# Performance work log

Hardware: AMD Instinct MI355X
Metric: run time of the kernel (lower is better)

## Reference

```python
import jax, jax.numpy as jnp
import numpy as np

B, N, E, H, D, MS, FF = 4, 500, 128, 8, 16, 16, 512
SQRT_D = 4.0  # sqrt_qkv_dim
EPS = 1e-5


def setup_inputs() -> dict:
    key = jax.random.key(0)
    ks = jax.random.split(key, 26)
    u = lambda k, sh, s: jax.random.uniform(k, sh, jnp.float32, -s, s)
    inp = {
        "x_edges_values": jax.random.uniform(ks[0], (B, N, N), jnp.float32),
        "depot_node_demand": jax.random.uniform(ks[1], (B, N, 1), jnp.float32),
        "rand": jax.random.uniform(ks[2], (B, E), jnp.float32),
        # attention projections (no bias)
        "Wq": u(ks[3], (E, H * D), E ** -0.5),
        "Wk": u(ks[4], (E, H * D), E ** -0.5),
        "Wv": u(ks[5], (E, H * D), E ** -0.5),
        # mixed-score per-head MLP
        "mix1_w": u(ks[6], (H, 2, MS), 0.7071067811865476),
        "mix1_b": u(ks[7], (H, MS), 0.7071067811865476),
        "mix2_w": u(ks[8], (H, MS, 1), 0.25),
        "mix2_b": u(ks[9], (H, 1), 0.25),
        # multi_head_combine
        "Wo": u(ks[10], (H * D, E), (H * D) ** -0.5),
        "bo": u(ks[11], (E,), (H * D) ** -0.5),
        # feed-forward
        "W1": u(ks[12], (E, FF), E ** -0.5),
        "b1": u(ks[13], (FF,), E ** -0.5),
        "W2": u(ks[14], (FF, E), FF ** -0.5),
        "b2": u(ks[15], (E,), FF ** -0.5),
        # batch norms (affine)
        "bn1_g": jnp.ones((E,), jnp.float32),
        "bn1_b": jnp.zeros((E,), jnp.float32),
        "bn2_g": jnp.ones((E,), jnp.float32),
        "bn2_b": jnp.zeros((E,), jnp.float32),
        # demand / node embeddings
        "Wd": u(ks[16], (1, E), 1.0),
        "bd": u(ks[17], (E,), 1.0),
        "Wn": u(ks[18], (2 * E, E), (2 * E) ** -0.5),
        "bn_node": u(ks[19], (E,), (2 * E) ** -0.5),
    }
    return inp


def _batchnorm(x, g, b):
    # BatchNorm1d in training mode over flattened [B*N, E]
    x2 = x.reshape(-1, E)
    m = x2.mean(0)
    v = ((x2 - m) ** 2).mean(0)  # biased variance, as torch uses for normalization
    return (((x2 - m) / jnp.sqrt(v + EPS)) * g + b).reshape(x.shape)


def reference(x_edges_values, depot_node_demand, rand, Wq, Wk, Wv,
              mix1_w, mix1_b, mix2_w, mix2_b, Wo, bo, W1, b1, W2, b2,
              bn1_g, bn1_b, bn2_g, bn2_b, Wd, bd, Wn, bn_node):
    # seed embeddings: row_emb zeros, col_emb scattered one-hot from a random perm
    row_emb = jnp.zeros((B, N, E), jnp.float32)
    perm = jnp.argsort(rand, axis=1)                       # [B, E] (seed_cnt = E since N > E)
    idx = jnp.concatenate([perm, perm, perm, perm], 1)[:, :N]  # 3E <= N < 4E branch
    col_emb = jax.nn.one_hot(idx, E, dtype=jnp.float32)    # [B, N, E]

    heads = lambda x: x.reshape(B, N, H, D).transpose(0, 2, 1, 3)  # [B,H,N,D]
    q = heads(row_emb @ Wq)
    k = heads(col_emb @ Wk)
    v = heads(col_emb @ Wv)

    dot = jnp.einsum('bhnd,bhmd->bhnm', q, k) / SQRT_D        # [B,H,N,N]
    cost = jnp.broadcast_to(x_edges_values[:, None], (B, H, N, N))
    two = jnp.stack([dot, cost], axis=-1)                      # [B,H,N,N,2]
    ms1 = jax.nn.relu(jnp.einsum('bhnmt,hts->bhnms', two, mix1_w)
                      + mix1_b[None, :, None, None, :])        # [B,H,N,N,MS]
    ms2 = jnp.einsum('bhnms,hso->bhnmo', ms1, mix2_w)[..., 0] \
          + mix2_b[None, :, None, :]                           # [B,H,N,N]
    weights = jax.nn.softmax(ms2, axis=-1)
    out = jnp.einsum('bhnm,bhmd->bhnd', weights, v)
    out_concat = out.transpose(0, 2, 1, 3).reshape(B, N, H * D)

    multi_head_out = out_concat @ Wo + bo
    out1 = _batchnorm(row_emb + multi_head_out, bn1_g, bn1_b)
    ff = jax.nn.relu(out1 @ W1 + b1) @ W2 + b2
    out3 = _batchnorm(out1 + ff, bn2_g, bn2_b)

    demand_feature = depot_node_demand @ Wd + bd               # [B,N,E]
    node_feature = jnp.concatenate([out3, demand_feature], -1) @ Wn + bn_node
    return node_feature
```

## Files before the change

### kernel.cpp

```cpp
#include <hip/hip_runtime.h>
#include <hip/hip_bf16.h>


#define BN_EPS 1e-5f
#define WS_X1    256000
#define WS_X2    512000
#define WS_SUM1  768000
#define WS_SQ1   768128
#define WS_SUM2  768256
#define WS_SQ2   768384
#define WS_UV    768512
#define WS_C0V   768640

#define GEMM_BATCH8(WPTR, LDW, KIDX, ACT2D, ACC)                        \
  {                                                                     \
    float4 w[8];                                                        \
    _Pragma("unroll")                                                   \
    for (int u = 0; u < 8; ++u)                                         \
      w[u] = *(const float4*)((WPTR) + (size_t)((KIDX) + u) * (LDW));   \
    _Pragma("unroll")                                                   \
    for (int u = 0; u < 8; ++u) {                                       \
      _Pragma("unroll")                                                 \
      for (int r = 0; r < 4; ++r) {                                     \
        float a = ACT2D[r][u];                                          \
        ACC[r][0] = fmaf(a, w[u].x, ACC[r][0]);                         \
        ACC[r][1] = fmaf(a, w[u].y, ACC[r][1]);                         \
        ACC[r][2] = fmaf(a, w[u].z, ACC[r][2]);                         \
        ACC[r][3] = fmaf(a, w[u].w, ACC[r][3]);                         \
      }                                                                 \
    }                                                                   \
  }

#define LOAD_ACT8(SRC2D, KIDX, ACT2D)                                   \
  {                                                                     \
    _Pragma("unroll")                                                   \
    for (int r = 0; r < 4; ++r) {                                       \
      float4 x = *(const float4*)&SRC2D[r][(KIDX)];                     \
      float4 y = *(const float4*)&SRC2D[r][(KIDX) + 4];                 \
      ACT2D[r][0] = x.x; ACT2D[r][1] = x.y; ACT2D[r][2] = x.z;          \
      ACT2D[r][3] = x.w; ACT2D[r][4] = y.x; ACT2D[r][5] = y.y;          \
      ACT2D[r][6] = y.z; ACT2D[r][7] = y.w;                             \
    }                                                                   \
  }

#define GB8_R2(WPTR, LDW, KIDX, ACT2D, ACC)                             \
  {                                                                     \
    float4 w[8];                                                        \
    _Pragma("unroll")                                                   \
    for (int u = 0; u < 8; ++u)                                         \
      w[u] = *(const float4*)((WPTR) + (size_t)((KIDX) + u) * (LDW));   \
    _Pragma("unroll")                                                   \
    for (int u = 0; u < 8; ++u) {                                       \
      _Pragma("unroll")                                                 \
      for (int r = 0; r < 2; ++r) {                                     \
        float a = ACT2D[r][u];                                          \
        ACC[r][0] = fmaf(a, w[u].x, ACC[r][0]);                         \
        ACC[r][1] = fmaf(a, w[u].y, ACC[r][1]);                         \
        ACC[r][2] = fmaf(a, w[u].z, ACC[r][2]);                         \
        ACC[r][3] = fmaf(a, w[u].w, ACC[r][3]);                         \
      }                                                                 \
    }                                                                   \
  }

#define LD_AV2(SRC_ROW0, SRC_ROW1, KIDX, ACT2D)                         \
  {                                                                     \
    float4 x0 = *(const float4*)&(SRC_ROW0)[(KIDX)];                    \
    float4 y0 = *(const float4*)&(SRC_ROW0)[(KIDX) + 4];                \
    float4 x1 = *(const float4*)&(SRC_ROW1)[(KIDX)];                    \
    float4 y1 = *(const float4*)&(SRC_ROW1)[(KIDX) + 4];                \
    ACT2D[0][0]=x0.x; ACT2D[0][1]=x0.y; ACT2D[0][2]=x0.z; ACT2D[0][3]=x0.w; \
    ACT2D[0][4]=y0.x; ACT2D[0][5]=y0.y; ACT2D[0][6]=y0.z; ACT2D[0][7]=y0.w; \
    ACT2D[1][0]=x1.x; ACT2D[1][1]=x1.y; ACT2D[1][2]=x1.z; ACT2D[1][3]=x1.w; \
    ACT2D[1][4]=y1.x; ACT2D[1][5]=y1.y; ACT2D[1][6]=y1.z; ACT2D[1][7]=y1.w; \
  }

__global__ __launch_bounds__(512, 4) void k_attn(const float* __restrict__ cost,
                                                 const float* __restrict__ rnd,
                                                 const float* __restrict__ Wv,
                                                 const float* __restrict__ mix1w,
                                                 const float* __restrict__ mix1b,
                                                 const float* __restrict__ mix2w,
                                                 const float* __restrict__ mix2b,
                                                 const float* __restrict__ Wo,
                                                 const float* __restrict__ bo,
                                                 float* __restrict__ ws) {
  __shared__ float scost[4][512];
  __shared__ float2 lut[8 * 256];
  __shared__ float aw[32][132];
  __shared__ float soc[4][132];
  __shared__ float sP[8][512];
  __shared__ float svr[128];
  __shared__ int   sperm[128];
  __shared__ float mu[8][16], mr[8][16], mA[8], mB[8];
  __shared__ float sS[512], sQ[512];
  const int t = threadIdx.x;
  const int lane = t & 63;
  const int blk = blockIdx.x;
  const int row0 = blk * 4;
  const int b = blk / 125;

  {
    int rr = t >> 7, i4 = t & 127;
    *(float4*)&scost[rr][i4 * 4] = (i4 < 125)
        ? *(const float4*)(cost + (size_t)(row0 + rr) * 500 + i4 * 4)
        : float4{0.f, 0.f, 0.f, 0.f};
  }
  if (t < 128) svr[t] = rnd[b * 128 + t];
  __syncthreads();
  if (t < 128) {
    float vt = svr[t];
    int rank = 0;
    for (int j = 0; j < 128; ++j) {
      float vj = svr[j];
      rank += (vj < vt) || (vj == vt && j < t);
    }
    sperm[rank] = t;
    int h = t >> 4, s = t & 15;
    float w1  = mix1w[h * 32 + 16 + s];
    float b1v = mix1b[h * 16 + s];
    float w2  = mix2w[h * 16 + s];
    bool tiny = fabsf(w1) < 1e-20f;
    float us = tiny ? 0.f : 0.5f * w2 * fabsf(w1);
    float rs = tiny ? 0.f : -b1v / w1;
    float Ap = 0.5f * w2 * w1;
    float Bp = 0.5f * w2 * b1v + (tiny ? 0.5f * w2 * fabsf(b1v) : 0.f);
    mu[h][s] = us; mr[h][s] = rs;
#pragma unroll
    for (int off = 1; off < 16; off <<= 1) {
      Ap += __shfl_xor(Ap, off);
      Bp += __shfl_xor(Bp, off);
    }
    if (s == 0) { mA[h] = Ap; mB[h] = Bp + mix2b[h]; }
  }
  __syncthreads();
  float* traw = &sP[0][0];
  if (t < 257) {
    float x = (float)t * (1.f / 255.f);
    for (int h = 0; h < 8; ++h) {
      float g = fmaf(x, mA[h], mB[h]);
#pragma unroll
      for (int s = 0; s < 16; ++s)
        g = fmaf(fabsf(x - mr[h][s]), mu[h][s], g);
      traw[h * 257 + t] = __expf(g);
    }
  }
  __syncthreads();
#pragma unroll
  for (int p = 0; p < 4; ++p) {
    int e = t + p * 512;
    int h = e >> 8, i = e & 255;
    float a = traw[h * 257 + i];
    lut[e] = float2{a, traw[h * 257 + i + 1] - a};
  }
  __syncthreads();
  {
    const int wid = t >> 6;
    const int r  = wid & 3;
    const int h0 = (wid >> 2) * 4;
    float cv8[8];
#pragma unroll
    for (int ii = 0; ii < 8; ++ii) cv8[ii] = scost[r][ii * 64 + lane];
    for (int h = h0; h < h0 + 4; ++h) {
      const float2* lh = &lut[h * 256];
      float wsum = 0.f, a0 = 0.f, a1 = 0.f;
#pragma unroll
      for (int ii = 0; ii < 8; ++ii) {
        float u = cv8[ii] * 255.f;
        int i = (int)u;
        float f = u - (float)i;
        float2 td = lh[i];
        float e = fmaf(td.y, f, td.x);
        if (ii == 7 && lane >= 52) e = 0.f;
        wsum += e;
        if (ii & 1) a1 += e; else a0 += e;
      }
#pragma unroll
      for (int off = 32; off; off >>= 1) wsum += __shfl_xor(wsum, off);
      float inv = 1.f / wsum;
      aw[r * 8 + h][lane]      = a0 * inv;
      aw[r * 8 + h][64 + lane] = a1 * inv;
    }
  }
  __syncthreads();
  {
    const int c  = t & 127;
    const int jh = t >> 7;
    const int h  = c >> 4;
    float acc4[4] = {0.f, 0.f, 0.f, 0.f};
    for (int jb = jh * 32; jb < jh * 32 + 32; jb += 8) {
      int rows[8];
#pragma unroll
      for (int u = 0; u < 8; ++u) rows[u] = sperm[jb + u];
      float wv8[8];
#pragma unroll
      for (int u = 0; u < 8; ++u) wv8[u] = Wv[(size_t)rows[u] * 128 + c];
#pragma unroll
      for (int r = 0; r < 4; ++r) {
        float4 aa = *(const float4*)&aw[r * 8 + h][jb];
        float4 ab = *(const float4*)&aw[r * 8 + h][jb + 4];
        acc4[r] = fmaf(aa.x, wv8[0], acc4[r]);
        acc4[r] = fmaf(aa.y, wv8[1], acc4[r]);
        acc4[r] = fmaf(aa.z, wv8[2], acc4[r]);
        acc4[r] = fmaf(aa.w, wv8[3], acc4[r]);
        acc4[r] = fmaf(ab.x, wv8[4], acc4[r]);
        acc4[r] = fmaf(ab.y, wv8[5], acc4[r]);
        acc4[r] = fmaf(ab.z, wv8[6], acc4[r]);
        acc4[r] = fmaf(ab.w, wv8[7], acc4[r]);
      }
    }
#pragma unroll
    for (int r = 0; r < 4; ++r) sP[jh][r * 128 + c] = acc4[r];
  }
  __syncthreads();
  {
    int r = t >> 7, c = t & 127;
    soc[r][c] = sP[0][r * 128 + c] + sP[1][r * 128 + c] +
                sP[2][r * 128 + c] + sP[3][r * 128 + c];
  }
  __syncthreads();
  {
    const int cg  = (t & 31) * 4;
    const int seg = (t >> 5) & 7;
    const int rh  = t >> 8;
    const int k0  = seg * 16;
    float acc[2][4] = {};
    float av[2][8];
#pragma unroll
    for (int kb = 0; kb < 16; kb += 8) {
      LD_AV2(soc[rh * 2], soc[rh * 2 + 1], k0 + kb, av);
      GB8_R2(Wo + cg, 128, k0 + kb, av, acc);
    }
#pragma unroll
    for (int r = 0; r < 2; ++r)
      *(float4*)&sP[seg][(rh * 2 + r) * 128 + cg] = *(float4*)acc[r];
  }
  __syncthreads();
  {
    int r = t >> 7, col = t & 127;
    float x = bo[col];
#pragma unroll
    for (int sg = 0; sg < 8; ++sg) x += sP[sg][r * 128 + col];
    ws[WS_X1 + (size_t)(row0 + r) * 128 + col] = x;
    sS[t] = x; sQ[t] = x * x;
  }
  __syncthreads();
  if (t < 128) {
    atomicAdd(ws + WS_SUM1 + t, sS[t] + sS[t+128] + sS[t+256] + sS[t+384]);
    atomicAdd(ws + WS_SQ1 + t, sQ[t] + sQ[t+128] + sQ[t+256] + sQ[t+384]);
  }
}

__global__ __launch_bounds__(512) void k_ffn(const float* __restrict__ W1,
                                             const float* __restrict__ b1,
                                             const float* __restrict__ g1,
                                             const float* __restrict__ bb1,
                                             const float* __restrict__ W2,
                                             const float* __restrict__ b2,
                                             const float* __restrict__ Wn,
                                             const float* __restrict__ Wd,
                                             const float* __restrict__ bd,
                                             const float* __restrict__ bnn,
                                             float* __restrict__ ws) {
  __shared__ float o1[8][128];
  __shared__ float sY[8][512];
  __shared__ float sP2[8][8][128];
  __shared__ float sS[512], sQ[512];
  const int t = threadIdx.x;
  const int row0 = blockIdx.x * 8;
  const int c0 = t & 127;
  float m1 = ws[WS_SUM1 + c0] * 5e-4f;
  float v1 = ws[WS_SQ1 + c0] * 5e-4f - m1 * m1;
  float scv = g1[c0] * rsqrtf(v1 + BN_EPS);
  float shv = bb1[c0] - m1 * scv;
  {
    int r0 = t >> 7;
    o1[r0][c0]     = ws[WS_X1 + (size_t)(row0 + r0) * 128 + c0] * scv + shv;
    o1[r0 + 4][c0] = ws[WS_X1 + (size_t)(row0 + r0 + 4) * 128 + c0] * scv + shv;
  }
  __syncthreads();
  {
    const int cg   = (t & 127) * 4;
    const int kseg = (t >> 7) & 1;
    const int rh   = t >> 8;
    const int kb0  = kseg * 64;
    float acc[4][4] = {};
    float av[4][8];
#pragma unroll
    for (int k0 = 0; k0 < 64; k0 += 8) {
      LOAD_ACT8((o1 + rh * 4), kb0 + k0, av);
      GEMM_BATCH8(W1 + cg, 512, kb0 + k0, av, acc);
    }
    float* pf = &sP2[0][0][0];
    if (kseg == 1) {
#pragma unroll
      for (int r = 0; r < 4; ++r)
        *(float4*)(pf + (size_t)(rh * 4 + r) * 512 + cg) = *(float4*)acc[r];
    }
    __syncthreads();
    if (kseg == 0) {
      float4 bv = *(const float4*)(b1 + cg);
#pragma unroll
      for (int r = 0; r < 4; ++r) {
        float4 p = *(float4*)(pf + (size_t)(rh * 4 + r) * 512 + cg);
        float4 y = {fmaxf(acc[r][0] + p.x + bv.x, 0.f),
                    fmaxf(acc[r][1] + p.y + bv.y, 0.f),
                    fmaxf(acc[r][2] + p.z + bv.z, 0.f),
                    fmaxf(acc[r][3] + p.w + bv.w, 0.f)};
        *(float4*)&sY[rh * 4 + r][cg] = y;
      }
    }
  }
  __syncthreads();
  {
    const int cg   = (t & 31) * 4;
    const int kseg = (t >> 5) & 7;
    const int rh   = t >> 8;
    const int k0   = kseg * 64;
    float acc[4][4] = {};
    float av[4][8];
#pragma unroll
    for (int kb = 0; kb < 64; kb += 8) {
      LOAD_ACT8((sY + rh * 4), k0 + kb, av);
      GEMM_BATCH8(W2 + cg, 128, k0 + kb, av, acc);
    }
#pragma unroll
    for (int r = 0; r < 4; ++r)
      *(float4*)&sP2[kseg][rh * 4 + r][cg] = *(float4*)acc[r];
  }
  __syncthreads();
  float s = 0.f, q = 0.f;
#pragma unroll
  for (int pass = 0; pass < 2; ++pass) {
    int idx = t + pass * 512;
    int col = idx & 127, r = idx >> 7;
    float x = b2[col] + o1[r][col];
#pragma unroll
    for (int sg = 0; sg < 8; ++sg) x += sP2[sg][r][col];
    ws[WS_X2 + (size_t)(row0 + r) * 128 + col] = x;
    s += x; q = fmaf(x, x, q);
  }
  sS[t] = s; sQ[t] = q;
  __syncthreads();
  if (t < 128) {
    atomicAdd(ws + WS_SUM2 + t, sS[t] + sS[t+128] + sS[t+256] + sS[t+384]);
    atomicAdd(ws + WS_SQ2 + t, sQ[t] + sQ[t+128] + sQ[t+256] + sQ[t+384]);
  }
  if (blockIdx.x == 0) {
    const int g = t >> 7;
    float u = 0.f, cc = 0.f;
#pragma unroll 8
    for (int e = g * 32; e < g * 32 + 32; ++e) {
      float wn = Wn[(size_t)(128 + e) * 128 + c0];
      u  = fmaf(Wd[e], wn, u);
      cc = fmaf(bd[e], wn, cc);
    }
    float* red = &sY[0][0];
    red[g * 128 + c0] = u;
    red[512 + g * 128 + c0] = cc;
    __syncthreads();
    if (t < 128) {
      ws[WS_UV + t]  = red[t] + red[128 + t] + red[256 + t] + red[384 + t];
      ws[WS_C0V + t] = red[512 + t] + red[640 + t] + red[768 + t] +
                       red[896 + t] + bnn[t];
    }
  }
}

__global__ __launch_bounds__(512, 4) void k_final(const float* __restrict__ Wn,
                                                  const float* __restrict__ g2,
                                                  const float* __restrict__ bb2,
                                                  const float* __restrict__ dem,
                                                  float* __restrict__ out,
                                                  float* __restrict__ ws) {
  __shared__ float o3[4][132];
  __shared__ float sP[8][4][128];
  const int t = threadIdx.x;
  const int row0 = blockIdx.x * 4;
  const int c0 = t & 127;
  float m2 = ws[WS_SUM2 + c0] * 5e-4f;
  float v2 = ws[WS_SQ2 + c0] * 5e-4f - m2 * m2;
  float scv = g2[c0] * rsqrtf(v2 + BN_EPS);
  float shv = bb2[c0] - m2 * scv;
  {
    int r = t >> 7;
    o3[r][c0] = ws[WS_X2 + (size_t)(row0 + r) * 128 + c0] * scv + shv;
  }
  __syncthreads();
  {
    const int cg  = (t & 31) * 4;
    const int seg = (t >> 5) & 7;
    const int rh  = t >> 8;
    const int k0  = seg * 16;
    float acc[2][4] = {};
    float av[2][8];
#pragma unroll
    for (int kb = 0; kb < 16; kb += 8) {
      LD_AV2(o3[rh * 2], o3[rh * 2 + 1], k0 + kb, av);
      GB8_R2(Wn + cg, 128, k0 + kb, av, acc);
    }
#pragma unroll
    for (int r = 0; r < 2; ++r)
      *(float4*)&sP[seg][rh * 2 + r][cg] = *(float4*)acc[r];
  }
  __syncthreads();
  {
    int r = t >> 7;
    float x = ws[WS_C0V + c0] + dem[row0 + r] * ws[WS_UV + c0];
#pragma unroll
    for (int sg = 0; sg < 8; ++sg) x += sP[sg][r][c0];
    out[(size_t)(row0 + r) * 128 + c0] = x;
  }
}

extern "C" void kernel_launch(void* const* d_in, const int* in_sizes, int n_in,
                              void* d_out, int out_size, void* d_ws, size_t ws_size,
                              hipStream_t stream) {
  const float* cost   = (const float*)d_in[0];
  const float* dem    = (const float*)d_in[1];
  const float* rnd    = (const float*)d_in[2];
  const float* Wv     = (const float*)d_in[5];
  const float* mix1w  = (const float*)d_in[6];
  const float* mix1b  = (const float*)d_in[7];
  const float* mix2w  = (const float*)d_in[8];
  const float* mix2b  = (const float*)d_in[9];
  const float* Wo     = (const float*)d_in[10];
  const float* bo     = (const float*)d_in[11];
  const float* W1     = (const float*)d_in[12];
  const float* b1     = (const float*)d_in[13];
  const float* W2     = (const float*)d_in[14];
  const float* b2     = (const float*)d_in[15];
  const float* g1     = (const float*)d_in[16];
  const float* bb1    = (const float*)d_in[17];
  const float* g2     = (const float*)d_in[18];
  const float* bb2    = (const float*)d_in[19];
  const float* Wd     = (const float*)d_in[20];
  const float* bd     = (const float*)d_in[21];
  const float* Wn     = (const float*)d_in[22];
  const float* bnn    = (const float*)d_in[23];
  float* ws  = (float*)d_ws;
  float* out = (float*)d_out;

  hipMemsetAsync(ws + WS_SUM1, 0, 512 * sizeof(float), stream);
  hipLaunchKernelGGL(k_attn,  dim3(500), dim3(512), 0, stream, cost, rnd, Wv,
                     mix1w, mix1b, mix2w, mix2b, Wo, bo, ws);
  hipLaunchKernelGGL(k_ffn,   dim3(250), dim3(512), 0, stream, W1, b1, g1, bb1,
                     W2, b2, Wn, Wd, bd, bnn, ws);
  hipLaunchKernelGGL(k_final, dim3(500), dim3(512), 0, stream, Wn, g2, bb2, dem,
                     out, ws);
}
```

Baseline: 54.81 us.

## Replace BN stat atomics with per-block partials and reduction kernels; retile FFN GEMMs

Batch-norm sum and square-sum statistics are now written as per-block partial slots and reduced by a new small reduction kernel launched between stages, instead of global atomicAdd plus a memset. The demand/Wn precompute moves from block 0 of the FFN kernel into that reduction kernel. The FFN GEMMs are retiled so each thread covers all 8 rows with a shorter k-slice (4 k-segments for W1, 16 for W2), with partial sums combined in shared memory. This trades atomics and the memset for two extra kernel launches, more shared memory and lower occupancy in the FFN kernel.

```diff
diff --git a/kernel.cpp b/kernel.cpp
--- a/kernel.cpp
+++ b/kernel.cpp
@@ -11,37 +11,8 @@
 #define WS_SQ2   768384
 #define WS_UV    768512
 #define WS_C0V   768640
-
-#define GEMM_BATCH8(WPTR, LDW, KIDX, ACT2D, ACC)                        \
-  {                                                                     \
-    float4 w[8];                                                        \
-    _Pragma("unroll")                                                   \
-    for (int u = 0; u < 8; ++u)                                         \
-      w[u] = *(const float4*)((WPTR) + (size_t)((KIDX) + u) * (LDW));   \
-    _Pragma("unroll")                                                   \
-    for (int u = 0; u < 8; ++u) {                                       \
-      _Pragma("unroll")                                                 \
-      for (int r = 0; r < 4; ++r) {                                     \
-        float a = ACT2D[r][u];                                          \
-        ACC[r][0] = fmaf(a, w[u].x, ACC[r][0]);                         \
-        ACC[r][1] = fmaf(a, w[u].y, ACC[r][1]);                         \
-        ACC[r][2] = fmaf(a, w[u].z, ACC[r][2]);                         \
-        ACC[r][3] = fmaf(a, w[u].w, ACC[r][3]);                         \
-      }                                                                 \
-    }                                                                   \
-  }
-
-#define LOAD_ACT8(SRC2D, KIDX, ACT2D)                                   \
-  {                                                                     \
-    _Pragma("unroll")                                                   \
-    for (int r = 0; r < 4; ++r) {                                       \
-      float4 x = *(const float4*)&SRC2D[r][(KIDX)];                     \
-      float4 y = *(const float4*)&SRC2D[r][(KIDX) + 4];                 \
-      ACT2D[r][0] = x.x; ACT2D[r][1] = x.y; ACT2D[r][2] = x.z;          \
-      ACT2D[r][3] = x.w; ACT2D[r][4] = y.x; ACT2D[r][5] = y.y;          \
-      ACT2D[r][6] = y.z; ACT2D[r][7] = y.w;                             \
-    }                                                                   \
-  }
+#define BN1P     770000
+#define BN2P     900000
 
 #define GB8_R2(WPTR, LDW, KIDX, ACT2D, ACC)                             \
   {                                                                     \
@@ -72,6 +43,30 @@
     ACT2D[0][4]=y0.x; ACT2D[0][5]=y0.y; ACT2D[0][6]=y0.z; ACT2D[0][7]=y0.w; \
     ACT2D[1][0]=x1.x; ACT2D[1][1]=x1.y; ACT2D[1][2]=x1.z; ACT2D[1][3]=x1.w; \
     ACT2D[1][4]=y1.x; ACT2D[1][5]=y1.y; ACT2D[1][6]=y1.z; ACT2D[1][7]=y1.w; \
+  }
+
+#define GB4_R8(WPTR, LDW, K0, SRC2D, ACC)                               \
+  {                                                                     \
+    float4 w[4];                                                        \
+    _Pragma("unroll")                                                   \
+    for (int u = 0; u < 4; ++u)                                         \
+      w[u] = *(const float4*)((WPTR) + (size_t)((K0) + u) * (LDW));     \
+    float av[8][4];                                                     \
+    _Pragma("unroll")                                                   \
+    for (int r = 0; r < 8; ++r) {                                       \
+      float4 x = *(const float4*)&SRC2D[r][(K0)];                       \
+      av[r][0] = x.x; av[r][1] = x.y; av[r][2] = x.z; av[r][3] = x.w;   \
+    }                                                                   \
+    _Pragma("unroll")                                                   \
+    for (int u = 0; u < 4; ++u) {                                       \
+      _Pragma("unroll")                                                 \
+      for (int r = 0; r < 8; ++r) {                                     \
+        ACC[r][0] = fmaf(av[r][u], w[u].x, ACC[r][0]);                  \
+        ACC[r][1] = fmaf(av[r][u], w[u].y, ACC[r][1]);                  \
+        ACC[r][2] = fmaf(av[r][u], w[u].z, ACC[r][2]);                  \
+        ACC[r][3] = fmaf(av[r][u], w[u].w, ACC[r][3]);                  \
+      }                                                                 \
+    }                                                                   \
   }
 
 __global__ __launch_bounds__(512, 4) void k_attn(const float* __restrict__ cost,
@@ -245,25 +240,61 @@
   }
   __syncthreads();
   if (t < 128) {
-    atomicAdd(ws + WS_SUM1 + t, sS[t] + sS[t+128] + sS[t+256] + sS[t+384]);
-    atomicAdd(ws + WS_SQ1 + t, sQ[t] + sQ[t+128] + sQ[t+256] + sQ[t+384]);
+    ws[BN1P + blk * 256 + t]       = sS[t] + sS[t+128] + sS[t+256] + sS[t+384];
+    ws[BN1P + blk * 256 + 128 + t] = sQ[t] + sQ[t+128] + sQ[t+256] + sQ[t+384];
   }
 }
 
-__global__ __launch_bounds__(512) void k_ffn(const float* __restrict__ W1,
-                                             const float* __restrict__ b1,
-                                             const float* __restrict__ g1,
-                                             const float* __restrict__ bb1,
-                                             const float* __restrict__ W2,
-                                             const float* __restrict__ b2,
-                                             const float* __restrict__ Wn,
+__global__ __launch_bounds__(256) void k_red(const float* __restrict__ Wn,
                                              const float* __restrict__ Wd,
                                              const float* __restrict__ bd,
                                              const float* __restrict__ bnn,
-                                             float* __restrict__ ws) {
+                                             float* __restrict__ ws,
+                                             int src, int nslots, int dst) {
+  const int t = threadIdx.x;
+  if (blockIdx.x < 8) {
+    __shared__ float red[8][33];
+    const int col = blockIdx.x * 32 + (t & 31);
+    const int strip = t >> 5;
+    float s = 0.f;
+    for (int j = strip; j < nslots; j += 8) s += ws[src + j * 256 + col];
+    red[strip][t & 31] = s;
+    __syncthreads();
+    if (t < 32) {
+      float x = 0.f;
+#pragma unroll
+      for (int k = 0; k < 8; ++k) x += red[k][t];
+      ws[dst + blockIdx.x * 32 + t] = x;
+    }
+  } else {
+    __shared__ float ru[2][128], rc[2][128];
+    const int c = t & 127, g = t >> 7;
+    float u = 0.f, cc = 0.f;
+#pragma unroll 8
+    for (int e = g * 64; e < g * 64 + 64; ++e) {
+      float wn = Wn[(size_t)(128 + e) * 128 + c];
+      u  = fmaf(Wd[e], wn, u);
+      cc = fmaf(bd[e], wn, cc);
+    }
+    ru[g][c] = u; rc[g][c] = cc;
+    __syncthreads();
+    if (t < 128) {
+      ws[WS_UV + t]  = ru[0][t] + ru[1][t];
+      ws[WS_C0V + t] = rc[0][t] + rc[1][t] + bnn[t];
+    }
+  }
+}
+
+__global__ __launch_bounds__(512, 2) void k_ffn(const float* __restrict__ W1,
+                                                const float* __restrict__ b1,
+                                                const float* __restrict__ g1,
+                                                const float* __restrict__ bb1,
+                                                const float* __restrict__ W2,
+                                                const float* __restrict__ b2,
+                                                float* __restrict__ ws) {
   __shared__ float o1[8][128];
   __shared__ float sY[8][512];
-  __shared__ float sP2[8][8][128];
+  __shared__ float sP[16][8][128];
   __shared__ float sS[512], sQ[512];
   const int t = threadIdx.x;
   const int row0 = blockIdx.x * 8;
@@ -278,91 +309,60 @@
     o1[r0 + 4][c0] = ws[WS_X1 + (size_t)(row0 + r0 + 4) * 128 + c0] * scv + shv;
   }
   __syncthreads();
+  float* p1 = &sP[0][0][0];
   {
     const int cg   = (t & 127) * 4;
-    const int kseg = (t >> 7) & 1;
-    const int rh   = t >> 8;
-    const int kb0  = kseg * 64;
-    float acc[4][4] = {};
-    float av[4][8];
-#pragma unroll
-    for (int k0 = 0; k0 < 64; k0 += 8) {
-      LOAD_ACT8((o1 + rh * 4), kb0 + k0, av);
-      GEMM_BATCH8(W1 + cg, 512, kb0 + k0, av, acc);
-    }
-    float* pf = &sP2[0][0][0];
-    if (kseg == 1) {
-#pragma unroll
-      for (int r = 0; r < 4; ++r)
-        *(float4*)(pf + (size_t)(rh * 4 + r) * 512 + cg) = *(float4*)acc[r];
-    }
-    __syncthreads();
-    if (kseg == 0) {
-      float4 bv = *(const float4*)(b1 + cg);
-#pragma unroll
-      for (int r = 0; r < 4; ++r) {
-        float4 p = *(float4*)(pf + (size_t)(rh * 4 + r) * 512 + cg);
-        float4 y = {fmaxf(acc[r][0] + p.x + bv.x, 0.f),
-                    fmaxf(acc[r][1] + p.y + bv.y, 0.f),
-                    fmaxf(acc[r][2] + p.z + bv.z, 0.f),
-                    fmaxf(acc[r][3] + p.w + bv.w, 0.f)};
-        *(float4*)&sY[rh * 4 + r][cg] = y;
-      }
-    }
+    const int kseg = t >> 7;
+    const int kb0  = kseg * 32;
+    float acc[8][4] = {};
+#pragma unroll
+    for (int kb = 0; kb < 32; kb += 4)
+      GB4_R8(W1 + cg, 512, kb0 + kb, (o1 + 0), acc);
+#pragma unroll
+    for (int r = 0; r < 8; ++r)
+      *(float4*)(p1 + (size_t)(kseg * 8 + r) * 512 + cg) = *(float4*)acc[r];
+  }
+  __syncthreads();
+#pragma unroll
+  for (int i = 0; i < 8; ++i) {
+    int idx = t + i * 512;
+    int r = idx >> 9, c = idx & 511;
+    float x = p1[(size_t)r * 512 + c] + p1[(size_t)(8 + r) * 512 + c] +
+              p1[(size_t)(16 + r) * 512 + c] + p1[(size_t)(24 + r) * 512 + c];
+    sY[r][c] = fmaxf(x + b1[c], 0.f);
   }
   __syncthreads();
   {
     const int cg   = (t & 31) * 4;
-    const int kseg = (t >> 5) & 7;
-    const int rh   = t >> 8;
-    const int k0   = kseg * 64;
-    float acc[4][4] = {};
-    float av[4][8];
-#pragma unroll
-    for (int kb = 0; kb < 64; kb += 8) {
-      LOAD_ACT8((sY + rh * 4), k0 + kb, av);
-      GEMM_BATCH8(W2 + cg, 128, k0 + kb, av, acc);
-    }
-#pragma unroll
-    for (int r = 0; r < 4; ++r)
-      *(float4*)&sP2[kseg][rh * 4 + r][cg] = *(float4*)acc[r];
+    const int kseg = t >> 5;
+    const int kb0  = kseg * 32;
+    float acc[8][4] = {};
+#pragma unroll
+    for (int kb = 0; kb < 32; kb += 4)
+      GB4_R8(W2 + cg, 128, kb0 + kb, (sY + 0), acc);
+#pragma unroll
+    for (int r = 0; r < 8; ++r)
+      *(float4*)&sP[kseg][r][cg] = *(float4*)acc[r];
   }
   __syncthreads();
   float s = 0.f, q = 0.f;
 #pragma unroll
   for (int pass = 0; pass < 2; ++pass) {
     int idx = t + pass * 512;
-    int col = idx & 127, r = idx >> 7;
-    float x = b2[col] + o1[r][col];
-#pragma unroll
-    for (int sg = 0; sg < 8; ++sg) x += sP2[sg][r][col];
-    ws[WS_X2 + (size_t)(row0 + r) * 128 + col] = x;
+    int r = idx >> 7, c = idx & 127;
+    float x = b2[c] + o1[r][c];
+#pragma unroll
+    for (int sg = 0; sg < 16; ++sg) x += sP[sg][r][c];
+    ws[WS_X2 + (size_t)(row0 + r) * 128 + c] = x;
     s += x; q = fmaf(x, x, q);
   }
   sS[t] = s; sQ[t] = q;
   __syncthreads();
   if (t < 128) {
-    atomicAdd(ws + WS_SUM2 + t, sS[t] + sS[t+128] + sS[t+256] + sS[t+384]);
-    atomicAdd(ws + WS_SQ2 + t, sQ[t] + sQ[t+128] + sQ[t+256] + sQ[t+384]);
-  }
-  if (blockIdx.x == 0) {
-    const int g = t >> 7;
-    float u = 0.f, cc = 0.f;
-#pragma unroll 8
-    for (int e = g * 32; e < g * 32 + 32; ++e) {
-      float wn = Wn[(size_t)(128 + e) * 128 + c0];
-      u  = fmaf(Wd[e], wn, u);
-      cc = fmaf(bd[e], wn, cc);
-    }
-    float* red = &sY[0][0];
-    red[g * 128 + c0] = u;
-    red[512 + g * 128 + c0] = cc;
-    __syncthreads();
-    if (t < 128) {
-      ws[WS_UV + t]  = red[t] + red[128 + t] + red[256 + t] + red[384 + t];
-      ws[WS_C0V + t] = red[512 + t] + red[640 + t] + red[768 + t] +
-                       red[896 + t] + bnn[t];
-    }
+    ws[BN2P + blockIdx.x * 256 + t] =
+        sS[t] + sS[t + 128] + sS[t + 256] + sS[t + 384];
+    ws[BN2P + blockIdx.x * 256 + 128 + t] =
+        sQ[t] + sQ[t + 128] + sQ[t + 256] + sQ[t + 384];
   }
 }
 
@@ -440,11 +440,14 @@
   float* ws  = (float*)d_ws;
   float* out = (float*)d_out;
 
-  hipMemsetAsync(ws + WS_SUM1, 0, 512 * sizeof(float), stream);
   hipLaunchKernelGGL(k_attn,  dim3(500), dim3(512), 0, stream, cost, rnd, Wv,
                      mix1w, mix1b, mix2w, mix2b, Wo, bo, ws);
+  hipLaunchKernelGGL(k_red,   dim3(9),   dim3(256), 0, stream, Wn, Wd, bd, bnn,
+                     ws, BN1P, 500, WS_SUM1);
   hipLaunchKernelGGL(k_ffn,   dim3(250), dim3(512), 0, stream, W1, b1, g1, bb1,
-                     W2, b2, Wn, Wd, bd, bnn, ws);
+                     W2, b2, ws);
+  hipLaunchKernelGGL(k_red,   dim3(8),   dim3(256), 0, stream, Wn, Wd, bd, bnn,
+                     ws, BN2P, 250, WS_SUM2);
   hipLaunchKernelGGL(k_final, dim3(500), dim3(512), 0, stream, Wn, g2, bb2, dem,
                      out, ws);
 }
```

Measured after the change: 64.42 us. 17.5% more time.
